# Kernel tuning notes

Hardware: AMD Instinct MI355X
Metric: run time of the kernel (lower is better)

The kernel has to match this reference:

```python
import jax, jax.numpy as jnp
import numpy as np

GN_EPS = 1e-5
NUM_GROUPS = 32


def setup_inputs() -> dict:
    key = jax.random.key(0)
    ks = jax.random.split(key, 4)
    B, K, N = 8192, 2048, 4096
    bound = 1.0 / np.sqrt(K)
    return {
        "x": jax.random.normal(ks[0], (B, K), dtype=jnp.float32),
        "weight": jax.random.normal(ks[1], (N, K), dtype=jnp.float32) * bound,
        "bias_lin": jax.random.uniform(ks[2], (N,), dtype=jnp.float32, minval=-bound, maxval=bound),
        "bias_extra": jax.random.normal(ks[3], (N,), dtype=jnp.float32),
        "gn_weight": jnp.ones((N,), dtype=jnp.float32),
        "gn_bias": jnp.zeros((N,), dtype=jnp.float32),
    }


def reference(x, weight, bias_lin, bias_extra, gn_weight, gn_bias):
    # Fused GEMM + bias + Swish + extra bias:  y = swish(x @ W.T + b_lin) + b_ex
    z = jnp.einsum("bk,nk->bn", x, weight) + bias_lin          # [B, N]
    y = z * jax.nn.sigmoid(z) + bias_extra                      # Swish + extra bias
    # GroupNorm over channel groups
    B, N = y.shape
    G = NUM_GROUPS
    yg = y.reshape(B, G, N // G)
    mean = jnp.mean(yg, axis=2, keepdims=True)
    var = jnp.mean(jnp.square(yg - mean), axis=2, keepdims=True)  # biased variance
    y_norm = ((yg - mean) * jax.lax.rsqrt(var + GN_EPS)).reshape(B, N)
    return y_norm * gn_weight + gn_bias
```

## Files before the change

### kernel.cpp

```cpp
#include <hip/hip_runtime.h>


typedef __attribute__((ext_vector_type(8))) short short8;
typedef __attribute__((ext_vector_type(4))) float f32x4;

#define M_DIM 8192
#define N_DIM 4096
#define K_DIM 2048
#define BM 128
#define BN 128
#define BK 64
#define NT (K_DIM / BK)

#define AS1 __attribute__((address_space(1)))
#define AS3 __attribute__((address_space(3)))

__global__ void f32_to_bf16_k(const float* __restrict__ in, ushort* __restrict__ out, int n8) {
    int i = blockIdx.x * blockDim.x + threadIdx.x;
    if (i >= n8) return;
    const float4* p = (const float4*)in + 2 * (size_t)i;
    float4 a = p[0], b = p[1];
    float v[8] = {a.x, a.y, a.z, a.w, b.x, b.y, b.z, b.w};
    ushort rr[8];
#pragma unroll
    for (int j = 0; j < 8; ++j) {
        unsigned u = __float_as_uint(v[j]);
        rr[j] = (ushort)((u + 0x7fffu + ((u >> 16) & 1u)) >> 16);
    }
    uint4 o;
    o.x = (unsigned)rr[0] | ((unsigned)rr[1] << 16);
    o.y = (unsigned)rr[2] | ((unsigned)rr[3] << 16);
    o.z = (unsigned)rr[4] | ((unsigned)rr[5] << 16);
    o.w = (unsigned)rr[6] | ((unsigned)rr[7] << 16);
    ((uint4*)out)[i] = o;
}


__global__ __launch_bounds__(256, 3) void gemm_swish_gn(
    const ushort* __restrict__ xb, const ushort* __restrict__ wb,
    const float* __restrict__ bias_lin, const float* __restrict__ bias_extra,
    const float* __restrict__ gn_w, const float* __restrict__ gn_b,
    float* __restrict__ out)
{
    extern __shared__ __align__(16) ushort lds[];

    const int t = threadIdx.x;
    const int w = t >> 6;
    const int l = t & 63;
    const int wm = w >> 1;
    const int wn = w & 1;
    const int h = l >> 4;
    const int r = l & 15;

    const int bid = blockIdx.x;
    const int xcd = bid & 7;
    const int pp = bid >> 3;
    const int brow = (xcd & 3) * 16 + (pp & 15);
    const int bcol = (xcd >> 2) * 16 + (pp >> 4);

    const int s = t >> 3;
    const int scol = (((t & 7) ^ (s & 7)) << 3);
    const ushort* pA = xb + (size_t)(brow * BM + s) * K_DIM + scol;
    const ushort* pB = wb + (size_t)(bcol * BN + s) * K_DIM + scol;
    const int dst = t * 8;

#define STG_A(ROFF) __builtin_amdgcn_global_load_lds(                          \
        (const AS1 void*)(pA + (size_t)(ROFF) * K_DIM),                        \
        (AS3 void*)&lds[(ROFF) * 64 + dst], 16, 0, 0)
#define STG_B(ROFF) __builtin_amdgcn_global_load_lds(                          \
        (const AS1 void*)(pB + (size_t)(ROFF) * K_DIM),                        \
        (AS3 void*)&lds[8192 + (ROFF) * 64 + dst], 16, 0, 0)

    const int xr8 = (r & 7) << 3;
    const int aOff0 = (wm * 64 + r) * 64 + ((h << 3) ^ xr8);
    const int aOff1 = aOff0 ^ 32;
    const int bOff0 = 8192 + (wn * 64 + r) * 64 + ((h << 3) ^ xr8);
    const int bOff1 = bOff0 ^ 32;

    f32x4 acc[4][4];
#pragma unroll
    for (int m = 0; m < 4; ++m)
#pragma unroll
        for (int n = 0; n < 4; ++n)
            acc[m][n] = f32x4{0.f, 0.f, 0.f, 0.f};

    short8 aF[4][2], bF[4][2];

#pragma unroll 1
    for (int kt = 0; kt < NT; ++kt) {
        STG_A(0); STG_A(32); STG_A(64); STG_A(96);
        STG_B(0); STG_B(32); STG_B(64); STG_B(96);
        pA += BK; pB += BK;
        __syncthreads();

#pragma unroll
        for (int m = 0; m < 4; ++m) {
            aF[m][0] = *(const short8*)&lds[aOff0 + m * 1024];
            aF[m][1] = *(const short8*)&lds[aOff1 + m * 1024];
        }
#pragma unroll
        for (int n = 0; n < 4; ++n) {
            bF[n][0] = *(const short8*)&lds[bOff0 + n * 1024];
            bF[n][1] = *(const short8*)&lds[bOff1 + n * 1024];
        }
#pragma unroll
        for (int kk = 0; kk < 2; ++kk)
#pragma unroll
            for (int m = 0; m < 4; ++m)
#pragma unroll
                for (int n = 0; n < 4; ++n)
                    acc[m][n] = __builtin_amdgcn_mfma_f32_16x16x32_bf16(
                        aF[m][kk], bF[n][kk], acc[m][n], 0, 0, 0);

        __syncthreads();
    }

    const int colbase = bcol * BN + wn * 64;
    float bl[4], be[4], gwv[4], gbv[4];
#pragma unroll
    for (int n = 0; n < 4; ++n) {
        int col = colbase + n * 16 + r;
        bl[n] = bias_lin[col];
        be[n] = bias_extra[col];
        gwv[n] = gn_w[col];
        gbv[n] = gn_b[col];
    }

    float s1[4][4], s2[4][4];
#pragma unroll
    for (int m = 0; m < 4; ++m)
#pragma unroll
        for (int j = 0; j < 4; ++j) { s1[m][j] = 0.f; s2[m][j] = 0.f; }

#pragma unroll
    for (int m = 0; m < 4; ++m)
#pragma unroll
        for (int n = 0; n < 4; ++n)
#pragma unroll
            for (int j = 0; j < 4; ++j) {
                float z = acc[m][n][j] + bl[n];
                float sw = z / (1.f + __expf(-z)) + be[n];
                acc[m][n][j] = sw;
                s1[m][j] += sw;
                s2[m][j] += sw * sw;
            }

#pragma unroll
    for (int mask = 1; mask < 16; mask <<= 1) {
#pragma unroll
        for (int m = 0; m < 4; ++m)
#pragma unroll
            for (int j = 0; j < 4; ++j) {
                s1[m][j] += __shfl_xor(s1[m][j], mask, 16);
                s2[m][j] += __shfl_xor(s2[m][j], mask, 16);
            }
    }

    float* sred = (float*)&lds[16384];
    if (r == 0) {
#pragma unroll
        for (int m = 0; m < 4; ++m)
#pragma unroll
            for (int j = 0; j < 4; ++j) {
                int row = wm * 64 + m * 16 + h * 4 + j;
                sred[(0 * 2 + wn) * 128 + row] = s1[m][j];
                sred[(1 * 2 + wn) * 128 + row] = s2[m][j];
            }
    }
    __syncthreads();

    const size_t orow0 = (size_t)brow * BM;
#pragma unroll
    for (int m = 0; m < 4; ++m)
#pragma unroll
        for (int j = 0; j < 4; ++j) {
            int row = wm * 64 + m * 16 + h * 4 + j;
            float mu = (sred[0 * 128 + row] + sred[1 * 128 + row]) * (1.f / 128.f);
            float ex2 = (sred[2 * 128 + row] + sred[3 * 128 + row]) * (1.f / 128.f);
            float var = ex2 - mu * mu;
            float rs = rsqrtf(var + 1e-5f);
            float* orow = out + (orow0 + row) * N_DIM;
#pragma unroll
            for (int n = 0; n < 4; ++n) {
                int col = colbase + n * 16 + r;
                orow[col] = (acc[m][n][j] - mu) * rs * gwv[n] + gbv[n];
            }
        }
}

extern "C" void kernel_launch(void* const* d_in, const int* in_sizes, int n_in,
                              void* d_out, int out_size, void* d_ws, size_t ws_size,
                              hipStream_t stream) {
    const float* x        = (const float*)d_in[0];
    const float* weight   = (const float*)d_in[1];
    const float* bias_lin = (const float*)d_in[2];
    const float* bias_ex  = (const float*)d_in[3];
    const float* gn_w     = (const float*)d_in[4];
    const float* gn_b     = (const float*)d_in[5];
    float* out = (float*)d_out;

    ushort* xb = (ushort*)d_ws;
    ushort* wb = xb + (size_t)M_DIM * K_DIM;

    {
        int n8 = (M_DIM * K_DIM) / 8;
        f32_to_bf16_k<<<n8 / 256, 256, 0, stream>>>(x, xb, n8);
    }
    {
        int n8 = (N_DIM * K_DIM) / 8;
        f32_to_bf16_k<<<n8 / 256, 256, 0, stream>>>(weight, wb, n8);
    }

    const size_t ldsB = 16384 * sizeof(ushort) + 512 * sizeof(float);
    dim3 grid((M_DIM / BM) * (N_DIM / BN));
    gemm_swish_gn<<<grid, 256, ldsB, stream>>>(xb, wb, bias_lin, bias_ex, gn_w, gn_b, out);
}
```

Measured before the change: 182.0 us.

## Switch GEMM inner loop to 32x32x16 bf16 MFMA with 2x2 accumulator tiles

Replaces the 4x4 grid of 16x16x32 MFMAs per wave with a 2x2 grid of 32x32x16 MFMAs. Each wave now issues fewer MFMA instructions and fewer LDS fragment loads per K-tile. The swizzled LDS read offsets, the epilogue row mapping and the GroupNorm shuffle reduction are rewritten to match the 32x32 accumulator layout. Launch bounds rise to 4 blocks per SM, which caps registers per thread and could cause spills.

```diff
diff --git a/kernel.cpp b/kernel.cpp
--- a/kernel.cpp
+++ b/kernel.cpp
@@ -2,7 +2,7 @@
 
 
 typedef __attribute__((ext_vector_type(8))) short short8;
-typedef __attribute__((ext_vector_type(4))) float f32x4;
+typedef __attribute__((ext_vector_type(16))) float f32x16;
 
 #define M_DIM 8192
 #define N_DIM 4096
@@ -36,7 +36,7 @@
 }
 
 
-__global__ __launch_bounds__(256, 3) void gemm_swish_gn(
+__global__ __launch_bounds__(256, 4) void gemm_swish_gn(
     const ushort* __restrict__ xb, const ushort* __restrict__ wb,
     const float* __restrict__ bias_lin, const float* __restrict__ bias_extra,
     const float* __restrict__ gn_w, const float* __restrict__ gn_b,
@@ -49,8 +49,8 @@
     const int l = t & 63;
     const int wm = w >> 1;
     const int wn = w & 1;
-    const int h = l >> 4;
-    const int r = l & 15;
+    const int r32 = l & 31;
+    const int hb = l >> 5;
 
     const int bid = blockIdx.x;
     const int xcd = bid & 7;
@@ -71,20 +71,20 @@
         (const AS1 void*)(pB + (size_t)(ROFF) * K_DIM),                        \
         (AS3 void*)&lds[8192 + (ROFF) * 64 + dst], 16, 0, 0)
 
-    const int xr8 = (r & 7) << 3;
-    const int aOff0 = (wm * 64 + r) * 64 + ((h << 3) ^ xr8);
-    const int aOff1 = aOff0 ^ 32;
-    const int bOff0 = 8192 + (wn * 64 + r) * 64 + ((h << 3) ^ xr8);
-    const int bOff1 = bOff0 ^ 32;
-
-    f32x4 acc[4][4];
-#pragma unroll
-    for (int m = 0; m < 4; ++m)
-#pragma unroll
-        for (int n = 0; n < 4; ++n)
-            acc[m][n] = f32x4{0.f, 0.f, 0.f, 0.f};
-
-    short8 aF[4][2], bF[4][2];
+    const int sw = r32 & 7;
+    const int e2 = sw & 6;
+    const int o1 = hb ^ (sw & 1);
+    const int aRow = (wm * 64 + r32) * 64;
+    const int bRow = 8192 + (wn * 64 + r32) * 64;
+
+    f32x16 acc[2][2];
+#pragma unroll
+    for (int mb = 0; mb < 2; ++mb)
+#pragma unroll
+        for (int nb = 0; nb < 2; ++nb)
+#pragma unroll
+            for (int i = 0; i < 16; ++i)
+                acc[mb][nb][i] = 0.f;
 
 #pragma unroll 1
     for (int kt = 0; kt < NT; ++kt) {
@@ -94,96 +94,83 @@
         __syncthreads();
 
 #pragma unroll
-        for (int m = 0; m < 4; ++m) {
-            aF[m][0] = *(const short8*)&lds[aOff0 + m * 1024];
-            aF[m][1] = *(const short8*)&lds[aOff1 + m * 1024];
-        }
-#pragma unroll
-        for (int n = 0; n < 4; ++n) {
-            bF[n][0] = *(const short8*)&lds[bOff0 + n * 1024];
-            bF[n][1] = *(const short8*)&lds[bOff1 + n * 1024];
-        }
-#pragma unroll
-        for (int kk = 0; kk < 2; ++kk)
-#pragma unroll
-            for (int m = 0; m < 4; ++m)
-#pragma unroll
-                for (int n = 0; n < 4; ++n)
-                    acc[m][n] = __builtin_amdgcn_mfma_f32_16x16x32_bf16(
-                        aF[m][kk], bF[n][kk], acc[m][n], 0, 0, 0);
+        for (int kq = 0; kq < 4; ++kq) {
+            const int slot8 = ((((kq << 1) ^ e2) | o1) << 3);
+            short8 aF0 = *(const short8*)&lds[aRow + slot8];
+            short8 aF1 = *(const short8*)&lds[aRow + 2048 + slot8];
+            short8 bF0 = *(const short8*)&lds[bRow + slot8];
+            short8 bF1 = *(const short8*)&lds[bRow + 2048 + slot8];
+            acc[0][0] = __builtin_amdgcn_mfma_f32_32x32x16_bf16(aF0, bF0, acc[0][0], 0, 0, 0);
+            acc[0][1] = __builtin_amdgcn_mfma_f32_32x32x16_bf16(aF0, bF1, acc[0][1], 0, 0, 0);
+            acc[1][0] = __builtin_amdgcn_mfma_f32_32x32x16_bf16(aF1, bF0, acc[1][0], 0, 0, 0);
+            acc[1][1] = __builtin_amdgcn_mfma_f32_32x32x16_bf16(aF1, bF1, acc[1][1], 0, 0, 0);
+        }
 
         __syncthreads();
     }
 
     const int colbase = bcol * BN + wn * 64;
-    float bl[4], be[4], gwv[4], gbv[4];
-#pragma unroll
-    for (int n = 0; n < 4; ++n) {
-        int col = colbase + n * 16 + r;
-        bl[n] = bias_lin[col];
-        be[n] = bias_extra[col];
-        gwv[n] = gn_w[col];
-        gbv[n] = gn_b[col];
-    }
-
-    float s1[4][4], s2[4][4];
-#pragma unroll
-    for (int m = 0; m < 4; ++m)
-#pragma unroll
-        for (int j = 0; j < 4; ++j) { s1[m][j] = 0.f; s2[m][j] = 0.f; }
-
-#pragma unroll
-    for (int m = 0; m < 4; ++m)
-#pragma unroll
-        for (int n = 0; n < 4; ++n)
-#pragma unroll
-            for (int j = 0; j < 4; ++j) {
-                float z = acc[m][n][j] + bl[n];
-                float sw = z / (1.f + __expf(-z)) + be[n];
-                acc[m][n][j] = sw;
-                s1[m][j] += sw;
-                s2[m][j] += sw * sw;
-            }
-
-#pragma unroll
-    for (int mask = 1; mask < 16; mask <<= 1) {
-#pragma unroll
-        for (int m = 0; m < 4; ++m)
-#pragma unroll
-            for (int j = 0; j < 4; ++j) {
-                s1[m][j] += __shfl_xor(s1[m][j], mask, 16);
-                s2[m][j] += __shfl_xor(s2[m][j], mask, 16);
-            }
+    float bl[2], be[2], gwv[2], gbv[2];
+#pragma unroll
+    for (int nb = 0; nb < 2; ++nb) {
+        int col = colbase + nb * 32 + r32;
+        bl[nb] = bias_lin[col];
+        be[nb] = bias_extra[col];
+        gwv[nb] = gn_w[col];
+        gbv[nb] = gn_b[col];
     }
 
     float* sred = (float*)&lds[16384];
-    if (r == 0) {
-#pragma unroll
-        for (int m = 0; m < 4; ++m)
-#pragma unroll
-            for (int j = 0; j < 4; ++j) {
-                int row = wm * 64 + m * 16 + h * 4 + j;
-                sred[(0 * 2 + wn) * 128 + row] = s1[m][j];
-                sred[(1 * 2 + wn) * 128 + row] = s2[m][j];
-            }
+
+#pragma unroll
+    for (int mb = 0; mb < 2; ++mb) {
+        float s1[16], s2[16];
+#pragma unroll
+        for (int i = 0; i < 16; ++i) { s1[i] = 0.f; s2[i] = 0.f; }
+#pragma unroll
+        for (int nb = 0; nb < 2; ++nb)
+#pragma unroll
+            for (int i = 0; i < 16; ++i) {
+                float z = acc[mb][nb][i] + bl[nb];
+                float swv = z / (1.f + __expf(-z)) + be[nb];
+                acc[mb][nb][i] = swv;
+                s1[i] += swv;
+                s2[i] += swv * swv;
+            }
+#pragma unroll
+        for (int mask = 1; mask < 32; mask <<= 1) {
+#pragma unroll
+            for (int i = 0; i < 16; ++i) {
+                s1[i] += __shfl_xor(s1[i], mask, 64);
+                s2[i] += __shfl_xor(s2[i], mask, 64);
+            }
+        }
+        if (r32 == 0) {
+#pragma unroll
+            for (int i = 0; i < 16; ++i) {
+                int row = wm * 64 + mb * 32 + (i & 3) + 8 * (i >> 2) + 4 * hb;
+                sred[(0 * 2 + wn) * 128 + row] = s1[i];
+                sred[(1 * 2 + wn) * 128 + row] = s2[i];
+            }
+        }
     }
     __syncthreads();
 
     const size_t orow0 = (size_t)brow * BM;
 #pragma unroll
-    for (int m = 0; m < 4; ++m)
-#pragma unroll
-        for (int j = 0; j < 4; ++j) {
-            int row = wm * 64 + m * 16 + h * 4 + j;
-            float mu = (sred[0 * 128 + row] + sred[1 * 128 + row]) * (1.f / 128.f);
-            float ex2 = (sred[2 * 128 + row] + sred[3 * 128 + row]) * (1.f / 128.f);
+    for (int mb = 0; mb < 2; ++mb)
+#pragma unroll
+        for (int i = 0; i < 16; ++i) {
+            int row = wm * 64 + mb * 32 + (i & 3) + 8 * (i >> 2) + 4 * hb;
+            float mu = (sred[row] + sred[128 + row]) * (1.f / 128.f);
+            float ex2 = (sred[256 + row] + sred[384 + row]) * (1.f / 128.f);
             float var = ex2 - mu * mu;
             float rs = rsqrtf(var + 1e-5f);
             float* orow = out + (orow0 + row) * N_DIM;
 #pragma unroll
-            for (int n = 0; n < 4; ++n) {
-                int col = colbase + n * 16 + r;
-                orow[col] = (acc[m][n][j] - mu) * rs * gwv[n] + gbv[n];
+            for (int nb = 0; nb < 2; ++nb) {
+                int col = colbase + nb * 32 + r32;
+                orow[col] = (acc[mb][nb][i] - mu) * rs * gwv[nb] + gbv[nb];
             }
         }
 }
```

After: 224.4 us. +23.3%, slower.
